# Kernel optimization log

Hardware: AMD Instinct MI355X
Metric: run time of the kernel (lower is better)

## Reference

```python
import jax, jax.numpy as jnp
import numpy as np

EMBED_DIM = 2048
NUM_HEADS = 32
NUM_KV_HEADS = 8
HEAD_DIM = EMBED_DIM // NUM_HEADS          # 64
GROUP = NUM_HEADS // NUM_KV_HEADS          # 4 queries per KV head
BATCH, SEQ = 2, 2048


def setup_inputs() -> dict:
    key = jax.random.key(0)
    ks = jax.random.split(key, 9)
    s_in = 1.0 / np.sqrt(EMBED_DIM)
    kv_dim = NUM_KV_HEADS * HEAD_DIM
    return {
        "x":      jax.random.normal(ks[0], (BATCH, SEQ, EMBED_DIM), jnp.float32),
        "Wq":     jax.random.normal(ks[1], (EMBED_DIM, EMBED_DIM), jnp.float32) * s_in,
        "bq":     jnp.zeros((EMBED_DIM,), jnp.float32),
        "Wk":     jax.random.normal(ks[2], (EMBED_DIM, kv_dim), jnp.float32) * s_in,
        "bk":     jnp.zeros((kv_dim,), jnp.float32),
        "Wv":     jax.random.normal(ks[3], (EMBED_DIM, kv_dim), jnp.float32) * s_in,
        "bv":     jnp.zeros((kv_dim,), jnp.float32),
        "Wo":     jax.random.normal(ks[4], (EMBED_DIM, EMBED_DIM), jnp.float32) * s_in,
        "bo":     jnp.zeros((EMBED_DIM,), jnp.float32),
    }


def reference(x, Wq, bq, Wk, bk, Wv, bv, Wo, bo):
    B, S, _ = x.shape
    # Projections (torch Linear == x @ W + b with W stored as [in, out] here)
    q = (x @ Wq + bq).reshape(B, S, NUM_KV_HEADS, GROUP, HEAD_DIM)  # grouped heads
    k = (x @ Wk + bk).reshape(B, S, NUM_KV_HEADS, HEAD_DIM)
    v = (x @ Wv + bv).reshape(B, S, NUM_KV_HEADS, HEAD_DIM)

    scale = 1.0 / np.sqrt(HEAD_DIM)
    # scores[b, h, g, s, t] = q[b, s, h, g, :] . k[b, t, h, :]
    # (repeat_interleave of K across the group dim == broadcasting over g)
    scores = jnp.einsum("bshgd,bthd->bhgst", q, k) * scale
    attn = jax.nn.softmax(scores, axis=-1)
    out = jnp.einsum("bhgst,bthd->bshgd", attn, v)  # [B, S, kvh, g, D]
    out = out.reshape(B, S, EMBED_DIM)
    return out @ Wo + bo
```

## Files before the change

kernel.cpp:

```cpp
#include <hip/hip_runtime.h>


typedef __attribute__((ext_vector_type(8)))  short     s16x8;
typedef __attribute__((ext_vector_type(8)))  _Float16  h8;
typedef __attribute__((ext_vector_type(2)))  __fp16    fp16x2;
typedef __attribute__((ext_vector_type(4)))  float     f32x4;
typedef __attribute__((ext_vector_type(16))) float     f32x16;

#define DEVI static __device__ __forceinline__

#if __has_builtin(__builtin_amdgcn_exp2f)
#define EXP2F __builtin_amdgcn_exp2f
#else
#define EXP2F exp2f
#endif

DEVI short f2h(float f){ _Float16 h = (_Float16)f; return __builtin_bit_cast(short, h); }
DEVI unsigned pkh(float a, float b){
  fp16x2 t = __builtin_amdgcn_cvt_pkrtz(a, b);
  return __builtin_bit_cast(unsigned, t);
}

typedef __attribute__((address_space(3))) unsigned       lds_u32;
typedef __attribute__((address_space(1))) const unsigned gbl_u32;
DEVI void glds16(const short* g, short* l){
  __builtin_amdgcn_global_load_lds((gbl_u32*)g, (lds_u32*)l, 16, 0, 0);
}

__global__ void cast_kernel(const float* __restrict__ in, short* __restrict__ out, int n){
  int i = (blockIdx.x * 256 + threadIdx.x) * 8;
  if(i >= n) return;
  float4 a = *(const float4*)(in + i);
  float4 b = *(const float4*)(in + i + 4);
  s16x8 v;
  v[0]=f2h(a.x); v[1]=f2h(a.y); v[2]=f2h(a.z); v[3]=f2h(a.w);
  v[4]=f2h(b.x); v[5]=f2h(b.y); v[6]=f2h(b.z); v[7]=f2h(b.w);
  *(s16x8*)(out + i) = v;
}

__global__ void prep_kernel(const float* __restrict__ Wq, const float* __restrict__ Wk,
                            const float* __restrict__ Wv, const float* __restrict__ Wo,
                            const float* __restrict__ bq, const float* __restrict__ bk,
                            const float* __restrict__ bv,
                            short* __restrict__ WT, short* __restrict__ WoT,
                            float* __restrict__ bqkv){
  __shared__ __align__(16) short tile[64*72];
  const int gy = blockIdx.y;
  const int t = threadIdx.x;
  if(gy >= 80){
    int i = blockIdx.x * 256 + t;
    if(i < 3072) bqkv[i] = (i < 2048) ? bq[i] : (i < 2560 ? bk[i-2048] : bv[i-2560]);
    return;
  }
  const float* src; short* dst; int ldin, by;
  if(gy < 32)      { src = Wq; dst = WT;             ldin = 2048; by = gy;    }
  else if(gy < 40) { src = Wk; dst = WT + 2048*2048; ldin =  512; by = gy-32; }
  else if(gy < 48) { src = Wv; dst = WT + 2560*2048; ldin =  512; by = gy-40; }
  else             { src = Wo; dst = WoT;            ldin = 2048; by = gy-48; }
  const int tr = blockIdx.x * 64;
  const int tc = by * 64;
  for(int c = t; c < 512; c += 256){
    int r = c >> 3, g = c & 7;
    const float* p = src + (size_t)(tr + r) * ldin + tc + g*8;
    s16x8 v;
    #pragma unroll
    for(int e = 0; e < 8; e++) v[e] = f2h(p[e]);
    *(s16x8*)&tile[r*72 + g*8] = v;
  }
  __syncthreads();
  for(int c = t; c < 512; c += 256){
    int r = c >> 3, g = c & 7;
    s16x8 v;
    #pragma unroll
    for(int e = 0; e < 8; e++) v[e] = tile[(g*8+e)*72 + r];
    *(s16x8*)(dst + (size_t)(tc + r) * 2048 + tr + g*8) = v;
  }
}

__global__ void transpose_h_kernel(const short* __restrict__ in, short* __restrict__ out,
                                   int ldin, int ldout){
  __shared__ __align__(16) short tile[64*72];
  const int tr = blockIdx.x * 64;
  const int tc = blockIdx.y * 64;
  const int t = threadIdx.x;
  for(int c = t; c < 512; c += 256){
    int r = c >> 3, g = c & 7;
    *(s16x8*)&tile[r*72 + g*8] = *(const s16x8*)(in + (size_t)(tr + r) * ldin + tc + g*8);
  }
  __syncthreads();
  for(int c = t; c < 512; c += 256){
    int r = c >> 3, g = c & 7;
    s16x8 v;
    #pragma unroll
    for(int e = 0; e < 8; e++) v[e] = tile[(g*8+e)*72 + r];
    *(s16x8*)(out + (size_t)(tc + r) * ldout + tr + g*8) = v;
  }
}

template<bool OUT_F32>
__global__ __launch_bounds__(256, 2)
void gemm_bt_kernel(const short* __restrict__ A, const short* __restrict__ BT,
                    const float* __restrict__ bias, void* __restrict__ C,
                    int M, int N, int K, int scale_cols, float qscale){
  __shared__ __align__(16) short As[128*32];
  __shared__ __align__(16) short Bs[128*32];
  const int m0 = blockIdx.x * 128;
  const int n0 = blockIdx.y * 128;
  const int tid = threadIdx.x;
  const int wave = tid >> 6, lane = tid & 63;
  const int l16 = lane & 15, quad = lane >> 4;
  const int wm = (wave >> 1) * 64, wn = (wave & 1) * 64;

  const short* gA = A  + (size_t)(m0 + wave*32 + (lane>>2))*K + (lane&3)*8;
  const short* gB = BT + (size_t)(n0 + wave*32 + (lane>>2))*K + (lane&3)*8;
  short* lA = As + wave*32*32;
  short* lB = Bs + wave*32*32;

  f32x4 acc[4][4];
  #pragma unroll
  for(int i=0;i<4;i++)
    #pragma unroll
    for(int j=0;j<4;j++) acc[i][j] = (f32x4)(0.0f);

  for(int k0 = 0; k0 < K; k0 += 32){
    glds16(gA + k0,                lA);
    glds16(gA + 16*(size_t)K + k0, lA + 512);
    glds16(gB + k0,                lB);
    glds16(gB + 16*(size_t)K + k0, lB + 512);
    __syncthreads();
    h8 af[4], bfr[4];
    #pragma unroll
    for(int i=0;i<4;i++){
      af[i]  = *(const h8*)&As[(wm + i*16 + l16)*32 + quad*8];
      bfr[i] = *(const h8*)&Bs[(wn + i*16 + l16)*32 + quad*8];
    }
    #pragma unroll
    for(int i=0;i<4;i++)
      #pragma unroll
      for(int j=0;j<4;j++)
        acc[i][j] = __builtin_amdgcn_mfma_f32_16x16x32_f16(af[i], bfr[j], acc[i][j], 0, 0, 0);
    __syncthreads();
  }

  #pragma unroll
  for(int j=0;j<4;j++){
    int col = n0 + wn + j*16 + l16;
    float bb = bias[col];
    float sc = (col < scale_cols) ? qscale : 1.0f;
    #pragma unroll
    for(int i=0;i<4;i++){
      #pragma unroll
      for(int r=0;r<4;r++){
        size_t row = (size_t)(m0 + wm + i*16 + quad*4 + r);
        float v = (acc[i][j][r] + bb) * sc;
        if(OUT_F32) ((float*)C)[row*(size_t)N + col] = v;
        else        ((short*)C)[row*(size_t)N + col] = f2h(v);
      }
    }
  }
}

__global__ __launch_bounds__(256, 2)
void attn_kernel(const short* __restrict__ Qg, const short* __restrict__ Kg,
                 const short* __restrict__ VT, short* __restrict__ Og, int ldq){
  const int qt  = blockIdx.x;
  const int kvh = blockIdx.y;
  const int b   = blockIdx.z;
  const int tid = threadIdx.x;
  const int wave = tid >> 6, lane = tid & 63;
  const int c = lane & 31, h = lane >> 5;
  const int head = kvh*4 + wave;
  const int q0 = qt * 64;

  __shared__ __align__(16) short Ks[2][64*72];
  __shared__ __align__(16) short Vs[2][64*72];

  h8 qreg[4][2];
  #pragma unroll
  for(int ks2=0; ks2<4; ks2++)
    #pragma unroll
    for(int qg=0; qg<2; qg++)
      qreg[ks2][qg] = *(const h8*)(Qg + (size_t)(b*2048 + q0 + qg*32 + c)*ldq
                                      + head*64 + ks2*16 + h*8);

  float lsum[2] = {0.0f, 0.0f};
  f32x16 oacc[2][2];
  #pragma unroll
  for(int qg=0; qg<2; qg++)
    #pragma unroll
    for(int mb=0; mb<2; mb++) oacc[qg][mb] = (f32x16)(0.0f);

  const short* gK = Kg + (size_t)(b*2048 + (tid>>3))*ldq + kvh*64 + (tid&7)*8;
  const short* gV = VT + (size_t)(kvh*64 + (tid>>3))*4096 + b*2048 + (tid&7)*8;
  const int so = (tid>>3)*72 + (tid&7)*8;
  const size_t kHalf = (size_t)32 * ldq;

  s16x8 kr0 = *(const s16x8*)(gK);
  s16x8 kr1 = *(const s16x8*)(gK + kHalf);
  s16x8 vr0 = *(const s16x8*)(gV);
  s16x8 vr1 = *(const s16x8*)(gV + 32*4096);

  for(int t0 = 0; t0 < 2048; t0 += 64){
    const int buf = (t0 >> 6) & 1;
    short* sK = &Ks[buf][so];
    short* sV = &Vs[buf][so];
    *(s16x8*)sK           = kr0;
    *(s16x8*)(sK + 32*72) = kr1;
    *(s16x8*)sV           = vr0;
    *(s16x8*)(sV + 32*72) = vr1;
    __syncthreads();
    if(t0 + 64 < 2048){
      const short* nK = gK + (size_t)(t0 + 64)*ldq;
      const short* nV = gV + (t0 + 64);
      kr0 = *(const s16x8*)(nK);
      kr1 = *(const s16x8*)(nK + kHalf);
      vr0 = *(const s16x8*)(nV);
      vr1 = *(const s16x8*)(nV + 32*4096);
    }
    const short* Kbuf = Ks[buf];
    const short* Vbuf = Vs[buf];

    #pragma unroll
    for(int kb=0; kb<2; kb++){
      f32x16 st[2];
      st[0] = (f32x16)(0.0f); st[1] = (f32x16)(0.0f);
      #pragma unroll
      for(int ks2=0; ks2<4; ks2++){
        h8 ak = *(const h8*)&Kbuf[(kb*32 + c)*72 + ks2*16 + h*8];
        st[0] = __builtin_amdgcn_mfma_f32_32x32x16_f16(ak, qreg[ks2][0], st[0], 0, 0, 0);
        st[1] = __builtin_amdgcn_mfma_f32_32x32x16_f16(ak, qreg[ks2][1], st[1], 0, 0, 0);
      }

      union H8U { h8 v; unsigned u[4]; };
      H8U pk[2][2];
      #pragma unroll
      for(int qg=0; qg<2; qg++){
        float sacc = 0.0f;
        #pragma unroll
        for(int j=0; j<4; j++){
          float pa = EXP2F(st[qg][2*j]);
          float pb = EXP2F(st[qg][2*j+1]);
          sacc += pa + pb;
          pk[qg][0].u[j] = pkh(pa, pb);
        }
        #pragma unroll
        for(int j=0; j<4; j++){
          float pa = EXP2F(st[qg][8+2*j]);
          float pb = EXP2F(st[qg][8+2*j+1]);
          sacc += pa + pb;
          pk[qg][1].u[j] = pkh(pa, pb);
        }
        lsum[qg] += sacc;
      }

      #pragma unroll
      for(int ksp=0; ksp<2; ksp++){
        #pragma unroll
        for(int mb=0; mb<2; mb++){
          const short* vb = &Vbuf[(mb*32 + c)*72 + kb*32 + ksp*16 + h*4];
          H8U av;
          *(uint2*)&av.u[0] = *(const uint2*)(vb);
          *(uint2*)&av.u[2] = *(const uint2*)(vb + 8);
          oacc[0][mb] = __builtin_amdgcn_mfma_f32_32x32x16_f16(av.v, pk[0][ksp].v, oacc[0][mb], 0, 0, 0);
          oacc[1][mb] = __builtin_amdgcn_mfma_f32_32x32x16_f16(av.v, pk[1][ksp].v, oacc[1][mb], 0, 0, 0);
        }
      }
    }
  }

  #pragma unroll
  for(int qg=0; qg<2; qg++){
    lsum[qg] += __shfl_xor(lsum[qg], 32);
    float li = 1.0f / lsum[qg];
    size_t rowoff = (size_t)(b*2048 + q0 + qg*32 + c)*2048 + head*64;
    #pragma unroll
    for(int mb=0; mb<2; mb++){
      #pragma unroll
      for(int g2=0; g2<4; g2++){
        int d0 = mb*32 + 8*g2 + 4*h;
        uint2 w;
        w.x = pkh(oacc[qg][mb][4*g2+0]*li, oacc[qg][mb][4*g2+1]*li);
        w.y = pkh(oacc[qg][mb][4*g2+2]*li, oacc[qg][mb][4*g2+3]*li);
        *(uint2*)&Og[rowoff + d0] = w;
      }
    }
  }
}

extern "C" void kernel_launch(void* const* d_in, const int* in_sizes, int n_in,
                              void* d_out, int out_size, void* d_ws, size_t ws_size,
                              hipStream_t stream){
  const float* x  = (const float*)d_in[0];
  const float* Wq = (const float*)d_in[1];
  const float* bq = (const float*)d_in[2];
  const float* Wk = (const float*)d_in[3];
  const float* bk = (const float*)d_in[4];
  const float* Wv = (const float*)d_in[5];
  const float* bv = (const float*)d_in[6];
  const float* Wo = (const float*)d_in[7];
  const float* bo = (const float*)d_in[8];

  char* ws = (char*)d_ws;
  short* WT   = (short*)(ws);
  short* WoT  = (short*)(ws + 25165824);
  short* xb   = (short*)(ws + 33554432);
  short* QKV  = (short*)(ws + 50331648);
  short* VTb  = (short*)(ws + 75497472);
  float* bqkv = (float*)(ws + 79691776);
  short* AO   = xb;

  cast_kernel<<<4096, 256, 0, stream>>>(x, xb, 8388608);
  prep_kernel<<<dim3(32,81), 256, 0, stream>>>(Wq, Wk, Wv, Wo, bq, bk, bv, WT, WoT, bqkv);

  gemm_bt_kernel<false><<<dim3(32,24), 256, 0, stream>>>(xb, WT, bqkv, QKV,
                                                         4096, 3072, 2048,
                                                         2048, 0.1803368801111244f);

  transpose_h_kernel<<<dim3(64,8), 256, 0, stream>>>(QKV + 2560, VTb, 3072, 4096);

  attn_kernel<<<dim3(32,8,2), 256, 0, stream>>>(QKV, QKV + 2048, VTb, AO, 3072);

  gemm_bt_kernel<true><<<dim3(32,16), 256, 0, stream>>>(AO, WoT, bo, (float*)d_out,
                                                        4096, 2048, 2048, 0, 1.0f);
}
```

Baseline: 303.0 us.

## Split attention key tile across two wave groups with LDS reduction

```diff
diff --git a/kernel.cpp b/kernel.cpp
--- a/kernel.cpp
+++ b/kernel.cpp
@@ -160,7 +160,7 @@
   }
 }
 
-__global__ __launch_bounds__(256, 2)
+__global__ __launch_bounds__(512, 4)
 void attn_kernel(const short* __restrict__ Qg, const short* __restrict__ Kg,
                  const short* __restrict__ VT, short* __restrict__ Og, int ldq){
   const int qt  = blockIdx.x;
@@ -169,11 +169,14 @@
   const int tid = threadIdx.x;
   const int wave = tid >> 6, lane = tid & 63;
   const int c = lane & 31, h = lane >> 5;
-  const int head = kvh*4 + wave;
+  const int hl = wave & 3, kb = wave >> 2;
+  const int head = kvh*4 + hl;
   const int q0 = qt * 64;
 
-  __shared__ __align__(16) short Ks[2][64*72];
-  __shared__ __align__(16) short Vs[2][64*72];
+  __shared__ __align__(16) short smem[4*64*72];
+  __shared__ float lsumS[4][2][64];
+  short* Ks = smem;
+  short* Vs = smem + 2*64*72;
 
   h8 qreg[4][2];
   #pragma unroll
@@ -190,98 +193,110 @@
     #pragma unroll
     for(int mb=0; mb<2; mb++) oacc[qg][mb] = (f32x16)(0.0f);
 
-  const short* gK = Kg + (size_t)(b*2048 + (tid>>3))*ldq + kvh*64 + (tid&7)*8;
-  const short* gV = VT + (size_t)(kvh*64 + (tid>>3))*4096 + b*2048 + (tid&7)*8;
-  const int so = (tid>>3)*72 + (tid&7)*8;
-  const size_t kHalf = (size_t)32 * ldq;
-
-  s16x8 kr0 = *(const s16x8*)(gK);
-  s16x8 kr1 = *(const s16x8*)(gK + kHalf);
-  s16x8 vr0 = *(const s16x8*)(gV);
-  s16x8 vr1 = *(const s16x8*)(gV + 32*4096);
+  const int srow = tid >> 3, spc = tid & 7;
+  const short* gK = Kg + (size_t)(b*2048 + srow)*ldq + kvh*64 + spc*8;
+  const short* gV = VT + (size_t)(kvh*64 + srow)*4096 + b*2048 + spc*8;
+  const int so = srow*72 + spc*8;
+
+  s16x8 kr = *(const s16x8*)(gK);
+  s16x8 vr = *(const s16x8*)(gV);
 
   for(int t0 = 0; t0 < 2048; t0 += 64){
     const int buf = (t0 >> 6) & 1;
-    short* sK = &Ks[buf][so];
-    short* sV = &Vs[buf][so];
-    *(s16x8*)sK           = kr0;
-    *(s16x8*)(sK + 32*72) = kr1;
-    *(s16x8*)sV           = vr0;
-    *(s16x8*)(sV + 32*72) = vr1;
+    *(s16x8*)&Ks[buf*64*72 + so] = kr;
+    *(s16x8*)&Vs[buf*64*72 + so] = vr;
     __syncthreads();
     if(t0 + 64 < 2048){
-      const short* nK = gK + (size_t)(t0 + 64)*ldq;
-      const short* nV = gV + (t0 + 64);
-      kr0 = *(const s16x8*)(nK);
-      kr1 = *(const s16x8*)(nK + kHalf);
-      vr0 = *(const s16x8*)(nV);
-      vr1 = *(const s16x8*)(nV + 32*4096);
-    }
-    const short* Kbuf = Ks[buf];
-    const short* Vbuf = Vs[buf];
-
-    #pragma unroll
-    for(int kb=0; kb<2; kb++){
-      f32x16 st[2];
-      st[0] = (f32x16)(0.0f); st[1] = (f32x16)(0.0f);
-      #pragma unroll
-      for(int ks2=0; ks2<4; ks2++){
-        h8 ak = *(const h8*)&Kbuf[(kb*32 + c)*72 + ks2*16 + h*8];
-        st[0] = __builtin_amdgcn_mfma_f32_32x32x16_f16(ak, qreg[ks2][0], st[0], 0, 0, 0);
-        st[1] = __builtin_amdgcn_mfma_f32_32x32x16_f16(ak, qreg[ks2][1], st[1], 0, 0, 0);
-      }
-
-      union H8U { h8 v; unsigned u[4]; };
-      H8U pk[2][2];
-      #pragma unroll
-      for(int qg=0; qg<2; qg++){
-        float sacc = 0.0f;
+      kr = *(const s16x8*)(gK + (size_t)(t0 + 64)*ldq);
+      vr = *(const s16x8*)(gV + (t0 + 64));
+    }
+    const short* Kbuf = Ks + buf*64*72;
+    const short* Vbuf = Vs + buf*64*72;
+
+    f32x16 st[2];
+    st[0] = (f32x16)(0.0f); st[1] = (f32x16)(0.0f);
+    #pragma unroll
+    for(int ks2=0; ks2<4; ks2++){
+      h8 ak = *(const h8*)&Kbuf[(kb*32 + c)*72 + ks2*16 + h*8];
+      st[0] = __builtin_amdgcn_mfma_f32_32x32x16_f16(ak, qreg[ks2][0], st[0], 0, 0, 0);
+      st[1] = __builtin_amdgcn_mfma_f32_32x32x16_f16(ak, qreg[ks2][1], st[1], 0, 0, 0);
+    }
+
+    union H8U { h8 v; unsigned u[4]; };
+    H8U pk[2][2];
+    #pragma unroll
+    for(int qg=0; qg<2; qg++){
+      float sacc = 0.0f;
+      #pragma unroll
+      for(int j=0; j<4; j++){
+        float pa = EXP2F(st[qg][2*j]);
+        float pb = EXP2F(st[qg][2*j+1]);
+        sacc += pa + pb;
+        pk[qg][0].u[j] = pkh(pa, pb);
+      }
+      #pragma unroll
+      for(int j=0; j<4; j++){
+        float pa = EXP2F(st[qg][8+2*j]);
+        float pb = EXP2F(st[qg][8+2*j+1]);
+        sacc += pa + pb;
+        pk[qg][1].u[j] = pkh(pa, pb);
+      }
+      lsum[qg] += sacc;
+    }
+
+    #pragma unroll
+    for(int ksp=0; ksp<2; ksp++){
+      #pragma unroll
+      for(int mb=0; mb<2; mb++){
+        const short* vb = &Vbuf[(mb*32 + c)*72 + kb*32 + ksp*16 + h*4];
+        H8U av;
+        *(uint2*)&av.u[0] = *(const uint2*)(vb);
+        *(uint2*)&av.u[2] = *(const uint2*)(vb + 8);
+        oacc[0][mb] = __builtin_amdgcn_mfma_f32_32x32x16_f16(av.v, pk[0][ksp].v, oacc[0][mb], 0, 0, 0);
+        oacc[1][mb] = __builtin_amdgcn_mfma_f32_32x32x16_f16(av.v, pk[1][ksp].v, oacc[1][mb], 0, 0, 0);
+      }
+    }
+  }
+
+  float* cm = (float*)smem;
+  #pragma unroll
+  for(int qg=0; qg<2; qg++){
+    __syncthreads();
+    if(kb == 1){
+      #pragma unroll
+      for(int mb=0; mb<2; mb++)
         #pragma unroll
-        for(int j=0; j<4; j++){
-          float pa = EXP2F(st[qg][2*j]);
-          float pb = EXP2F(st[qg][2*j+1]);
-          sacc += pa + pb;
-          pk[qg][0].u[j] = pkh(pa, pb);
+        for(int e=0; e<16; e++)
+          cm[((hl*2 + mb)*16 + e)*64 + lane] = oacc[qg][mb][e];
+      lsumS[hl][qg][lane] = lsum[qg];
+    }
+    __syncthreads();
+    if(kb == 0){
+      #pragma unroll
+      for(int mb=0; mb<2; mb++)
+        #pragma unroll
+        for(int e=0; e<16; e++)
+          oacc[qg][mb][e] += cm[((hl*2 + mb)*16 + e)*64 + lane];
+      lsum[qg] += lsumS[hl][qg][lane];
+    }
+  }
+
+  if(kb == 0){
+    #pragma unroll
+    for(int qg=0; qg<2; qg++){
+      lsum[qg] += __shfl_xor(lsum[qg], 32);
+      float li = 1.0f / lsum[qg];
+      size_t rowoff = (size_t)(b*2048 + q0 + qg*32 + c)*2048 + head*64;
+      #pragma unroll
+      for(int mb=0; mb<2; mb++){
+        #pragma unroll
+        for(int g2=0; g2<4; g2++){
+          int d0 = mb*32 + 8*g2 + 4*h;
+          uint2 w;
+          w.x = pkh(oacc[qg][mb][4*g2+0]*li, oacc[qg][mb][4*g2+1]*li);
+          w.y = pkh(oacc[qg][mb][4*g2+2]*li, oacc[qg][mb][4*g2+3]*li);
+          *(uint2*)&Og[rowoff + d0] = w;
         }
-        #pragma unroll
-        for(int j=0; j<4; j++){
-          float pa = EXP2F(st[qg][8+2*j]);
-          float pb = EXP2F(st[qg][8+2*j+1]);
-          sacc += pa + pb;
-          pk[qg][1].u[j] = pkh(pa, pb);
-        }
-        lsum[qg] += sacc;
-      }
-
-      #pragma unroll
-      for(int ksp=0; ksp<2; ksp++){
-        #pragma unroll
-        for(int mb=0; mb<2; mb++){
-          const short* vb = &Vbuf[(mb*32 + c)*72 + kb*32 + ksp*16 + h*4];
-          H8U av;
-          *(uint2*)&av.u[0] = *(const uint2*)(vb);
-          *(uint2*)&av.u[2] = *(const uint2*)(vb + 8);
-          oacc[0][mb] = __builtin_amdgcn_mfma_f32_32x32x16_f16(av.v, pk[0][ksp].v, oacc[0][mb], 0, 0, 0);
-          oacc[1][mb] = __builtin_amdgcn_mfma_f32_32x32x16_f16(av.v, pk[1][ksp].v, oacc[1][mb], 0, 0, 0);
-        }
-      }
-    }
-  }
-
-  #pragma unroll
-  for(int qg=0; qg<2; qg++){
-    lsum[qg] += __shfl_xor(lsum[qg], 32);
-    float li = 1.0f / lsum[qg];
-    size_t rowoff = (size_t)(b*2048 + q0 + qg*32 + c)*2048 + head*64;
-    #pragma unroll
-    for(int mb=0; mb<2; mb++){
-      #pragma unroll
-      for(int g2=0; g2<4; g2++){
-        int d0 = mb*32 + 8*g2 + 4*h;
-        uint2 w;
-        w.x = pkh(oacc[qg][mb][4*g2+0]*li, oacc[qg][mb][4*g2+1]*li);
-        w.y = pkh(oacc[qg][mb][4*g2+2]*li, oacc[qg][mb][4*g2+3]*li);
-        *(uint2*)&Og[rowoff + d0] = w;
       }
     }
   }
@@ -318,7 +333,7 @@
 
   transpose_h_kernel<<<dim3(64,8), 256, 0, stream>>>(QKV + 2560, VTb, 3072, 4096);
 
-  attn_kernel<<<dim3(32,8,2), 256, 0, stream>>>(QKV, QKV + 2048, VTb, AO, 3072);
+  attn_kernel<<<dim3(32,8,2), 512, 0, stream>>>(QKV, QKV + 2048, VTb, AO, 3072);
 
   gemm_bt_kernel<true><<<dim3(32,16), 256, 0, stream>>>(AO, WoT, bo, (float*)d_out,
                                                         4096, 2048, 2048, 0, 1.0f);
```

After: 421.9 us. 1.39x slower.
